# Performance work log

Hardware: AMD Instinct MI355X
Metric: run time of the kernel (lower is better)

Reference implementation:

```python
import jax, jax.numpy as jnp
import numpy as np

Nc, Np = 100_000, 200_000
E = 1_000_000
D_IN, C, H = 64, 128, 8
D = C // H  # per-head dim = 16
NEG_SLOPE = 0.2
BN_EPS = 1e-5


def setup_inputs() -> dict:
    key = jax.random.key(0)
    ks = jax.random.split(key, 24)
    rn = lambda i, shape, s=0.05: jax.random.normal(ks[i], shape, jnp.float32) * s
    inp = {
        'x_customer': jax.random.normal(ks[0], (Nc, D_IN), jnp.float32),
        'x_product': jax.random.normal(ks[1], (Np, D_IN), jnp.float32),
        'edge_src_cp': jax.random.randint(ks[2], (E,), 0, Nc),
        'edge_dst_cp': jax.random.randint(ks[3], (E,), 0, Np),
        'edge_src_pp': jax.random.randint(ks[4], (E,), 0, Np),
        'edge_dst_pp': jax.random.randint(ks[5], (E,), 0, Np),
        # HANConv per-node-type projections
        'W_c': rn(6, (D_IN, C)), 'b_c': jnp.zeros((C,), jnp.float32),
        'W_p': rn(7, (D_IN, C)), 'b_p': jnp.zeros((C,), jnp.float32),
        # per-edge-type attention vectors [H, D]
        'a_src_cp': rn(8, (H, D), 0.2), 'a_dst_cp': rn(9, (H, D), 0.2),
        'a_src_pp': rn(10, (H, D), 0.2), 'a_dst_pp': rn(11, (H, D), 0.2),
        # semantic attention (k_lin + q)
        'Wk': rn(12, (C, C)), 'bk': jnp.zeros((C,), jnp.float32),
        'q_sem': rn(13, (C,), 0.2),
        # MLP head + BN params
        'W1': rn(14, (C, 128)), 'b1': jnp.zeros((128,), jnp.float32),
        'g1': jnp.ones((128,), jnp.float32), 'be1': jnp.zeros((128,), jnp.float32),
        'W2': rn(15, (128, 64)), 'b2': jnp.zeros((64,), jnp.float32),
        'g2': jnp.ones((64,), jnp.float32), 'be2': jnp.zeros((64,), jnp.float32),
        'W3': rn(16, (64, 1)), 'b3': jnp.zeros((1,), jnp.float32),
    }
    return inp


def _edge_type_attention(h_src, h_dst, a_src, a_dst, e_src, e_dst, n_dst):
    # h_src: [N_src, H, D]; per-node attention logits [N, H]
    al_src = jnp.sum(h_src * a_src, axis=-1)
    al_dst = jnp.sum(h_dst * a_dst, axis=-1)
    al = al_src[e_src] + al_dst[e_dst]                      # [E, H]
    al = jnp.where(al >= 0, al, NEG_SLOPE * al)             # leaky_relu
    m = jax.ops.segment_max(al, e_dst, num_segments=n_dst)  # [n_dst, H]
    m = jnp.where(jnp.isfinite(m), m, 0.0)                  # empty segments
    ex = jnp.exp(al - m[e_dst])
    s = jax.ops.segment_sum(ex, e_dst, num_segments=n_dst)
    alpha = ex / (s[e_dst] + 1e-16)                         # [E, H]
    msg = h_src[e_src] * alpha[..., None]                   # [E, H, D]
    out = jax.ops.segment_sum(msg, e_dst, num_segments=n_dst)
    return jax.nn.relu(out.reshape(n_dst, H * D))


def _bn(x, g, b):
    mu = jnp.mean(x, axis=0)
    var = jnp.var(x, axis=0)
    return g * (x - mu) * jax.lax.rsqrt(var + BN_EPS) + b


def reference(x_customer, x_product, W_c, b_c, W_p, b_p,
              a_src_cp, a_dst_cp, a_src_pp, a_dst_pp,
              Wk, bk, q_sem,
              W1, b1, g1, be1, W2, b2, g2, be2, W3, b3,
              edge_src_cp, edge_dst_cp, edge_src_pp, edge_dst_pp):
    # node-type projections -> [N, H, D]
    h_c = (x_customer @ W_c + b_c).reshape(Nc, H, D)
    h_p = (x_product @ W_p + b_p).reshape(Np, H, D)
    # per-edge-type multi-head attention into 'product_order'
    out_cp = _edge_type_attention(h_c, h_p, a_src_cp, a_dst_cp, edge_src_cp, edge_dst_cp, Np)
    out_pp = _edge_type_attention(h_p, h_p, a_src_pp, a_dst_pp, edge_src_pp, edge_dst_pp, Np)
    # semantic attention over the 2 metapaths
    outs = jnp.stack([out_cp, out_pp])                      # [2, Np, C]
    k = jnp.mean(jnp.tanh(outs @ Wk + bk), axis=1)          # [2, C]
    attn = jax.nn.softmax(jnp.sum(k * q_sem, axis=-1))      # [2]
    out = jnp.sum(attn[:, None, None] * outs, axis=0)       # [Np, C]
    # MLP head (dropout disabled; BN uses batch statistics)
    h = jax.nn.relu(_bn(out @ W1 + b1, g1, be1))
    h = jax.nn.relu(_bn(h @ W2 + b2, g2, be2))
    return jax.nn.sigmoid(h @ W3 + b3)
```

## Files before the change

### kernel.cpp

```cpp
#include <hip/hip_runtime.h>
#include <hip/hip_bf16.h>

#define NC 100000
#define NP 200000
#define NE 1000000
#define NN2 (2 * NP)
#define NBUK 391
#define ECHUNK 8192
#define NBLK_E 245
#define NTILE 3125
#define NB8 391
#define NBLK_PC 391
#define NBLK_PP 782

typedef unsigned short u16;
typedef unsigned int u32;
typedef unsigned long long u64;
typedef __attribute__((ext_vector_type(8))) short short8v;
typedef __attribute__((ext_vector_type(4))) float f32x4;

__device__ __forceinline__ float bf2f(u16 v) {
    union { u32 u; float f; } c; c.u = ((u32)v) << 16; return c.f;
}
__device__ __forceinline__ u16 f2bf(float f) {
    union { float f; u32 u; } c; c.f = f;
    u32 u = c.u;
    return (u16)((u + 0x7FFFu + ((u >> 16) & 1u)) >> 16);
}
__device__ __forceinline__ u32 pack2(float lo, float hi) {
    return (u32)f2bf(lo) | ((u32)f2bf(hi) << 16);
}
__device__ __forceinline__ float tanh_fast(float x) {
    return 1.f - 2.f / (__expf(2.f * x) + 1.f);
}
__device__ __forceinline__ short8v mk8(u32 a, u32 b, u32 c, u32 d) {
    union { u32 u[4]; short8v v; } t; t.u[0] = a; t.u[1] = b; t.u[2] = c; t.u[3] = d; return t.v;
}

__global__ __launch_bounds__(256) void proj_both(
    const float* __restrict__ x_c, const float* __restrict__ W_c, const float* __restrict__ b_c,
    const float* __restrict__ x_p, const float* __restrict__ W_p, const float* __restrict__ b_p,
    u16* __restrict__ out_c, u16* __restrict__ out_p,
    const float* __restrict__ a_cp_s,
    const float* __restrict__ a_cp_d, const float* __restrict__ a_pp_s,
    const float* __restrict__ a_pp_d,
    float* __restrict__ al_c, float* __restrict__ al_dcp,
    float* __restrict__ al_spp, float* __restrict__ al_dpp,
    const int* __restrict__ dpp, const int* __restrict__ dcp, int* __restrict__ bcnt)
{
    __shared__ alignas(16) u16 sBT[128 * 72];
    __shared__ alignas(16) u16 hTile[64 * 136];
    __shared__ float aV[3][128];
    __shared__ int hh[NBUK];
    int t = threadIdx.x;
    int py = blockIdx.y;
    int bx = blockIdx.x;

    if (py == 0 && bx >= NBLK_PC) {
        int bb = bx - NBLK_PC;
        if (bb >= NBLK_E) return;
        for (int i = t; i < NBUK; i += 256) hh[i] = 0;
        __syncthreads();
        int base = bb * ECHUNK;
        int lim = min(ECHUNK, 2 * NE - base);
        for (int i = t; i < lim; i += 256) {
            int e = base + i;
            int d2 = (e < NE) ? dpp[e] : NP + dcp[e - NE];
            atomicAdd(&hh[d2 >> 10], 1);
        }
        __syncthreads();
        for (int i = t; i < NBUK; i += 256) if (hh[i]) atomicAdd(&bcnt[i], hh[i]);
        return;
    }

    const float* x; const float* W; const float* b; u16* h; int N;
    if (py == 0) { x = x_c; W = W_c; b = b_c; h = out_c; N = NC; }
    else         { x = x_p; W = W_p; b = b_p; h = out_p; N = NP; }
    if (t < 128) {
        aV[0][t] = py ? a_cp_d[t] : a_cp_s[t];
        aV[1][t] = py ? a_pp_s[t] : 0.f;
        aV[2][t] = py ? a_pp_d[t] : 0.f;
    }
    for (int i = t; i < 128 * 8; i += 256) {
        int n = i & 127, kb = i >> 7;
        u32 p[4];
#pragma unroll
        for (int j = 0; j < 4; ++j)
            p[j] = pack2(W[(kb * 8 + 2 * j) * 128 + n], W[(kb * 8 + 2 * j + 1) * 128 + n]);
        *(uint4*)(&sBT[n * 72 + kb * 8]) = make_uint4(p[0], p[1], p[2], p[3]);
    }
    __syncthreads();
    int wave = t >> 6, lane = t & 63;
    int fr = lane & 15, fq = lane >> 4;
    const u16* pB = sBT + fr * 72 + fq * 8;
    float bv8[8];
#pragma unroll
    for (int nt = 0; nt < 8; ++nt) bv8[nt] = b[nt * 16 + fr];

    for (int ti = 0; ti < 4; ++ti) {
        size_t row0 = ((size_t)bx * 4 + ti) * 64;
        if (row0 >= (size_t)N) break;
        size_t arow = row0 + wave * 16 + fr;
        short8v afr[2];
#pragma unroll
        for (int ks = 0; ks < 2; ++ks) {
            if (arow < (size_t)N) {
                const float* xp = x + arow * 64 + ks * 32 + fq * 8;
                float4 v0 = *(const float4*)xp;
                float4 v1 = *(const float4*)(xp + 4);
                afr[ks] = mk8(pack2(v0.x, v0.y), pack2(v0.z, v0.w),
                              pack2(v1.x, v1.y), pack2(v1.z, v1.w));
            } else afr[ks] = mk8(0, 0, 0, 0);
        }
        f32x4 acc[8];
#pragma unroll
        for (int nt = 0; nt < 8; ++nt) acc[nt] = (f32x4){bv8[nt], bv8[nt], bv8[nt], bv8[nt]};
#pragma unroll
        for (int ks = 0; ks < 2; ++ks) {
#pragma unroll
            for (int nt = 0; nt < 8; ++nt) {
                short8v bv = *(const short8v*)(pB + nt * 16 * 72 + ks * 32);
                acc[nt] = __builtin_amdgcn_mfma_f32_16x16x32_bf16(afr[ks], bv, acc[nt], 0, 0, 0);
            }
        }
        size_t rbase = row0 + wave * 16 + fq * 4;
        int lrow0 = wave * 16 + fq * 4;
#pragma unroll
        for (int nt = 0; nt < 8; ++nt) {
            int col = nt * 16 + fr;
#pragma unroll
            for (int rg = 0; rg < 4; ++rg) {
                size_t rr = rbase + rg;
                u16 hv = f2bf(acc[nt][rg]);
                if (rr < (size_t)N) h[rr * 128 + col] = hv;
                hTile[(lrow0 + rg) * 136 + col] = hv;
            }
        }
        __syncthreads();
        int row = t >> 2;
        size_t grow = row0 + row;
        if (grow < (size_t)N) {
#pragma unroll
            for (int hd = t & 3; hd < 8; hd += 4) {
                const u16* hp = &hTile[row * 136 + hd * 16];
                uint4 u0_ = *(const uint4*)hp;
                uint4 u1_ = *(const uint4*)(hp + 8);
                u32 uu[8] = {u0_.x, u0_.y, u0_.z, u0_.w, u1_.x, u1_.y, u1_.z, u1_.w};
                float p0 = 0.f, p1 = 0.f, p2 = 0.f;
#pragma unroll
                for (int j = 0; j < 8; ++j) {
                    float lo = bf2f((u16)(uu[j] & 0xFFFFu));
                    float hi = bf2f((u16)(uu[j] >> 16));
                    int c = hd * 16 + 2 * j;
                    p0 += lo * aV[0][c] + hi * aV[0][c + 1];
                    p1 += lo * aV[1][c] + hi * aV[1][c + 1];
                    p2 += lo * aV[2][c] + hi * aV[2][c + 1];
                }
                if (py == 0) {
                    al_c[grow * 8 + hd] = p0;
                } else {
                    al_dcp[grow * 8 + hd] = p0;
                    al_spp[grow * 8 + hd] = p1;
                    al_dpp[grow * 8 + hd] = p2;
                }
            }
        }
        __syncthreads();
    }
}

__global__ __launch_bounds__(512) void bscan(const int* __restrict__ bcnt, int* __restrict__ bbase,
                                             int* __restrict__ bcur, int* __restrict__ row_ptr)
{
    __shared__ int s[512];
    int t = threadIdx.x;
    int v = (t < NBUK) ? bcnt[t] : 0;
    s[t] = v;
    __syncthreads();
    for (int off = 1; off < 512; off <<= 1) {
        int x = (t >= off) ? s[t - off] : 0;
        __syncthreads();
        s[t] += x;
        __syncthreads();
    }
    if (t < NBUK) { bbase[t] = s[t] - v; bcur[t] = s[t] - v; }
    if (t == 0) { bbase[NBUK] = 2 * NE; row_ptr[NN2] = 2 * NE; }
}

__global__ __launch_bounds__(256) void bplace(
    const int* __restrict__ spp, const int* __restrict__ dpp,
    const int* __restrict__ scp, const int* __restrict__ dcp,
    int* __restrict__ bcur, u64* __restrict__ pairs)
{
    __shared__ int h[NBUK];
    __shared__ int rk[NBUK];
    int t = threadIdx.x;
    for (int i = t; i < NBUK; i += 256) h[i] = 0;
    __syncthreads();
    int base = blockIdx.x * ECHUNK;
    int lim = min(ECHUNK, 2 * NE - base);
    for (int i = t; i < lim; i += 256) {
        int e = base + i;
        int d2 = (e < NE) ? dpp[e] : NP + dcp[e - NE];
        atomicAdd(&h[d2 >> 10], 1);
    }
    __syncthreads();
    for (int i = t; i < NBUK; i += 256) {
        int c = h[i];
        h[i] = c ? atomicAdd(&bcur[i], c) : 0;
        rk[i] = 0;
    }
    __syncthreads();
    for (int i = t; i < lim; i += 256) {
        int e = base + i;
        int d2, src;
        if (e < NE) { d2 = dpp[e];      src = spp[e]; }
        else        { d2 = NP + dcp[e - NE]; src = scp[e - NE]; }
        int b = d2 >> 10;
        int r = atomicAdd(&rk[b], 1);
        pairs[h[b] + r] = ((u64)(u32)d2 << 32) | (u32)src;
    }
}

__global__ __launch_bounds__(256) void bsort(
    const u64* __restrict__ pairs, const int* __restrict__ bbase,
    int* __restrict__ row_ptr, int* __restrict__ perm)
{
    __shared__ int cnt[1024];
    __shared__ int sc[256];
    int b = blockIdx.x, t = threadIdx.x;
    int beg = bbase[b], end = bbase[b + 1];
    for (int i = t; i < 1024; i += 256) cnt[i] = 0;
    __syncthreads();
    for (int i = beg + t; i < end; i += 256) {
        int d2 = (int)(pairs[i] >> 32);
        atomicAdd(&cnt[d2 & 1023], 1);
    }
    __syncthreads();
    int b4 = t * 4;
    int c0 = cnt[b4], c1 = cnt[b4 + 1], c2 = cnt[b4 + 2], c3 = cnt[b4 + 3];
    int s = c0 + c1 + c2 + c3;
    sc[t] = s;
    __syncthreads();
    for (int off = 1; off < 256; off <<= 1) {
        int x = (t >= off) ? sc[t - off] : 0;
        __syncthreads();
        sc[t] += x;
        __syncthreads();
    }
    int run = sc[t] - s;
    int o0 = run, o1 = run + c0, o2 = o1 + c1, o3 = o2 + c2;
    cnt[b4] = o0; cnt[b4 + 1] = o1; cnt[b4 + 2] = o2; cnt[b4 + 3] = o3;
    int gidx = b * 1024 + b4;
    if (gidx     < NN2) row_ptr[gidx]     = beg + o0;
    if (gidx + 1 < NN2) row_ptr[gidx + 1] = beg + o1;
    if (gidx + 2 < NN2) row_ptr[gidx + 2] = beg + o2;
    if (gidx + 3 < NN2) row_ptr[gidx + 3] = beg + o3;
    __syncthreads();
    for (int i = beg + t; i < end; i += 256) {
        u64 p = pairs[i];
        int d2 = (int)(p >> 32);
        int r = atomicAdd(&cnt[d2 & 1023], 1);
        perm[beg + r] = (int)(p & 0xFFFFFFFFull);
    }
}

__global__ __launch_bounds__(256) void gather2(
    const int* __restrict__ row_ptr, const int* __restrict__ perm,
    const float* __restrict__ als_pp, const float* __restrict__ ald_pp,
    const float* __restrict__ als_cp, const float* __restrict__ ald_cp,
    const u16* __restrict__ h_p, const u16* __restrict__ h_c,
    u16* __restrict__ r_pp, u16* __restrict__ r_cp)
{
    int d2 = blockIdx.x * 16 + (threadIdx.x >> 4);
    int lane = threadIdx.x & 63;
    int l16 = lane & 15;
    int grp = lane & 48;
    int head = l16 >> 1;
    const float* als; const float* ald; const u16* hs; u16* out; int d;
    if (d2 < NP) { d = d2;      als = als_pp; ald = ald_pp; hs = h_p; out = r_pp; }
    else         { d = d2 - NP; als = als_cp; ald = ald_cp; hs = h_c; out = r_cp; }
    int beg = row_ptr[d2], end = row_ptr[d2 + 1];
    int n = end - beg;
    float ald_h = ald[(size_t)d * 8 + head];
    float dsum = 0.f;
    float acc[8] = {0.f, 0.f, 0.f, 0.f, 0.f, 0.f, 0.f, 0.f};
    for (int base = 0; base < n; base += 16) {
        int cnt = min(16, n - base);
        int my = (base + l16 < n) ? perm[beg + base + l16] : 0;
        int src = __shfl(my, grp, 64);
        float a_next = als[(size_t)src * 8 + head];
        uint4 hv_next = *(const uint4*)(hs + (size_t)src * 128 + l16 * 8);
        for (int j = 0; j < cnt; ++j) {
            float a_cur = a_next;
            uint4 hv = hv_next;
            if (j + 1 < cnt) {
                int s2 = __shfl(my, grp + j + 1, 64);
                a_next = als[(size_t)s2 * 8 + head];
                hv_next = *(const uint4*)(hs + (size_t)s2 * 128 + l16 * 8);
            }
            float a = a_cur + ald_h;
            a = a >= 0.f ? a : 0.2f * a;
            float w = __expf(a);
            dsum += w;
            u32 uu[4] = {hv.x, hv.y, hv.z, hv.w};
#pragma unroll
            for (int q = 0; q < 4; ++q) {
                acc[2 * q]     = fmaf(bf2f((u16)(uu[q] & 0xFFFFu)), w, acc[2 * q]);
                acc[2 * q + 1] = fmaf(bf2f((u16)(uu[q] >> 16)),     w, acc[2 * q + 1]);
            }
        }
    }
    float inv = 1.f / (dsum + 1e-16f);
    uint4 o;
    o.x = pack2(fmaxf(acc[0] * inv, 0.f), fmaxf(acc[1] * inv, 0.f));
    o.y = pack2(fmaxf(acc[2] * inv, 0.f), fmaxf(acc[3] * inv, 0.f));
    o.z = pack2(fmaxf(acc[4] * inv, 0.f), fmaxf(acc[5] * inv, 0.f));
    o.w = pack2(fmaxf(acc[6] * inv, 0.f), fmaxf(acc[7] * inv, 0.f));
    *(uint4*)(out + (size_t)d * 128 + l16 * 8) = o;
}

__global__ __launch_bounds__(256) void sem_mfma(
    const u16* __restrict__ r0, const u16* __restrict__ r1,
    const float* __restrict__ Wk, const float* __restrict__ bk,
    const float* __restrict__ q, float* __restrict__ vsum)
{
    __shared__ alignas(16) u16 sBT[128 * 136];
    __shared__ float red[4][128];
    __shared__ float sq_[128];
    __shared__ float dotb[128];
    int t = threadIdx.x;
    const u16* src = blockIdx.y ? r1 : r0;
    if (t < 128) sq_[t] = q[t];
    for (int i = t; i < 128 * 16; i += 256) {
        int n = i & 127, kb = i >> 7;
        u32 p[4];
#pragma unroll
        for (int j = 0; j < 4; ++j)
            p[j] = pack2(Wk[(kb * 8 + 2 * j) * 128 + n], Wk[(kb * 8 + 2 * j + 1) * 128 + n]);
        *(uint4*)(&sBT[n * 136 + kb * 8]) = make_uint4(p[0], p[1], p[2], p[3]);
    }
    __syncthreads();
    int wave = t >> 6, lane = t & 63;
    int fr = lane & 15, fq = lane >> 4;
    const u16* pB = sBT + fr * 136 + fq * 8;
    float bkv[8];
#pragma unroll
    for (int nt = 0; nt < 8; ++nt) bkv[nt] = bk[nt * 16 + fr];
    float sacc[8] = {0.f, 0.f, 0.f, 0.f, 0.f, 0.f, 0.f, 0.f};
    for (int ti = 0; ti < 8; ++ti) {
        int tile = blockIdx.x * 8 + ti;
        if (tile >= NTILE) break;
        size_t arow = (size_t)tile * 64 + wave * 16 + fr;
        const u16* ap = src + arow * 128 + fq * 8;
        short8v afr[4];
#pragma unroll
        for (int ks = 0; ks < 4; ++ks) afr[ks] = *(const short8v*)(ap + ks * 32);
        f32x4 acc[8];
#pragma unroll
        for (int nt = 0; nt < 8; ++nt) acc[nt] = (f32x4){bkv[nt], bkv[nt], bkv[nt], bkv[nt]};
#pragma unroll
        for (int ks = 0; ks < 4; ++ks) {
#pragma unroll
            for (int nt = 0; nt < 8; ++nt) {
                short8v bv = *(const short8v*)(pB + nt * 16 * 136 + ks * 32);
                acc[nt] = __builtin_amdgcn_mfma_f32_16x16x32_bf16(afr[ks], bv, acc[nt], 0, 0, 0);
            }
        }
#pragma unroll
        for (int nt = 0; nt < 8; ++nt) {
            f32x4 v = acc[nt];
            sacc[nt] += tanh_fast(v[0]) + tanh_fast(v[1]) + tanh_fast(v[2]) + tanh_fast(v[3]);
        }
    }
#pragma unroll
    for (int nt = 0; nt < 8; ++nt) {
        float s = sacc[nt];
        s += __shfl_xor(s, 16, 64);
        s += __shfl_xor(s, 32, 64);
        if (lane < 16) red[wave][nt * 16 + lane] = s;
    }
    __syncthreads();
    if (t < 128) dotb[t] = (red[0][t] + red[1][t] + red[2][t] + red[3][t]) * sq_[t];
    __syncthreads();
    if (t < 64) {
        float v = dotb[t] + dotb[t + 64];
#pragma unroll
        for (int off = 32; off >= 1; off >>= 1) v += __shfl_xor(v, off, 64);
        if (t == 0) atomicAdd(&vsum[blockIdx.y], v);
    }
}

__global__ __launch_bounds__(256) void mlp1_mfma(
    const u16* __restrict__ rcp, const u16* __restrict__ rpp, const float* __restrict__ vsum,
    const float* __restrict__ W1, const float* __restrict__ b1,
    u16* __restrict__ z1, float* __restrict__ pS, float* __restrict__ pQ)
{
    __shared__ alignas(16) u16 sBT[128 * 136];
    __shared__ float redS[4][128];
    __shared__ float redQ[4][128];
    int t = threadIdx.x;
    float v0 = vsum[0] * (1.f / (float)NP), v1 = vsum[1] * (1.f / (float)NP);
    float mx = fmaxf(v0, v1);
    float e0 = __expf(v0 - mx), e1 = __expf(v1 - mx);
    float is = 1.f / (e0 + e1);
    float a0 = e0 * is, a1 = e1 * is;
    for (int i = t; i < 128 * 16; i += 256) {
        int n = i & 127, kb = i >> 7;
        u32 p[4];
#pragma unroll
        for (int j = 0; j < 4; ++j)
            p[j] = pack2(W1[(kb * 8 + 2 * j) * 128 + n], W1[(kb * 8 + 2 * j + 1) * 128 + n]);
        *(uint4*)(&sBT[n * 136 + kb * 8]) = make_uint4(p[0], p[1], p[2], p[3]);
    }
    __syncthreads();
    int wave = t >> 6, lane = t & 63;
    int fr = lane & 15, fq = lane >> 4;
    const u16* pB = sBT + fr * 136 + fq * 8;
    float b1v[8];
#pragma unroll
    for (int nt = 0; nt < 8; ++nt) b1v[nt] = b1[nt * 16 + fr];
    float saccS[8] = {0.f, 0.f, 0.f, 0.f, 0.f, 0.f, 0.f, 0.f};
    float saccQ[8] = {0.f, 0.f, 0.f, 0.f, 0.f, 0.f, 0.f, 0.f};
    for (int ti = 0; ti < 8; ++ti) {
        int tile = blockIdx.x * 8 + ti;
        if (tile >= NTILE) break;
        size_t row0 = (size_t)tile * 64;
        size_t arow = row0 + wave * 16 + fr;
        const u16* rc = rcp + arow * 128 + fq * 8;
        const u16* rp = rpp + arow * 128 + fq * 8;
        f32x4 acc[8];
#pragma unroll
        for (int nt = 0; nt < 8; ++nt) acc[nt] = (f32x4){b1v[nt], b1v[nt], b1v[nt], b1v[nt]};
#pragma unroll
        for (int ks = 0; ks < 4; ++ks) {
            uint4 uc = *(const uint4*)(rc + ks * 32);
            uint4 up = *(const uint4*)(rp + ks * 32);
            u32 cu[4] = {uc.x, uc.y, uc.z, uc.w};
            u32 pu[4] = {up.x, up.y, up.z, up.w};
            u32 pw[4];
#pragma unroll
            for (int j = 0; j < 4; ++j) {
                float lo = a0 * bf2f((u16)(cu[j] & 0xFFFFu)) + a1 * bf2f((u16)(pu[j] & 0xFFFFu));
                float hi = a0 * bf2f((u16)(cu[j] >> 16))     + a1 * bf2f((u16)(pu[j] >> 16));
                pw[j] = pack2(lo, hi);
            }
            short8v a = mk8(pw[0], pw[1], pw[2], pw[3]);
#pragma unroll
            for (int nt = 0; nt < 8; ++nt) {
                short8v bv = *(const short8v*)(pB + nt * 16 * 136 + ks * 32);
                acc[nt] = __builtin_amdgcn_mfma_f32_16x16x32_bf16(a, bv, acc[nt], 0, 0, 0);
            }
        }
        size_t rbase = row0 + wave * 16 + fq * 4;
#pragma unroll
        for (int nt = 0; nt < 8; ++nt) {
            f32x4 v = acc[nt];
            int col = nt * 16 + fr;
#pragma unroll
            for (int rg = 0; rg < 4; ++rg)
                z1[(rbase + rg) * 128 + col] = f2bf(v[rg]);
            saccS[nt] += v[0] + v[1] + v[2] + v[3];
            saccQ[nt] += v[0] * v[0] + v[1] * v[1] + v[2] * v[2] + v[3] * v[3];
        }
    }
#pragma unroll
    for (int nt = 0; nt < 8; ++nt) {
        float s = saccS[nt], qq = saccQ[nt];
        s += __shfl_xor(s, 16, 64);  s += __shfl_xor(s, 32, 64);
        qq += __shfl_xor(qq, 16, 64); qq += __shfl_xor(qq, 32, 64);
        if (lane < 16) { redS[wave][nt * 16 + lane] = s; redQ[wave][nt * 16 + lane] = qq; }
    }
    __syncthreads();
    if (t < 128) {
        pS[(size_t)blockIdx.x * 128 + t] = redS[0][t] + redS[1][t] + redS[2][t] + redS[3][t];
        pQ[(size_t)blockIdx.x * 128 + t] = redQ[0][t] + redQ[1][t] + redQ[2][t] + redQ[3][t];
    }
}

__global__ __launch_bounds__(256) void stat_reduce(
    const float* __restrict__ pS, const float* __restrict__ pQ,
    float* __restrict__ sum, float* __restrict__ sq, int C)
{
    __shared__ float redS[256], redQ[256];
    int t = threadIdx.x;
    int c = t & (C - 1);
    int sub = t / C;
    int stride = 256 / C;
    int i0 = blockIdx.x * 25, i1 = i0 + 25;
    if (i1 > NB8) i1 = NB8;
    float s = 0.f, q = 0.f;
    for (int i = i0 + sub; i < i1; i += stride) {
        s += pS[(size_t)i * C + c];
        q += pQ[(size_t)i * C + c];
    }
    redS[t] = s; redQ[t] = q;
    __syncthreads();
    if (t < C) {
        for (int k = 1; k < stride; ++k) { s += redS[t + k * C]; q += redQ[t + k * C]; }
        atomicAdd(&sum[c], s);
        atomicAdd(&sq[c], q);
    }
}

__global__ __launch_bounds__(256) void mlp2_mfma(
    const u16* __restrict__ z1,
    const float* __restrict__ sum1, const float* __restrict__ sq1,
    const float* __restrict__ g1, const float* __restrict__ be1,
    const float* __restrict__ W2, const float* __restrict__ b2,
    u16* __restrict__ z2, float* __restrict__ pS, float* __restrict__ pQ)
{
    __shared__ alignas(16) u16 sBT[64 * 136];
    __shared__ float sSc[128], sSh[128];
    __shared__ float redS[4][64], redQ[4][64];
    int t = threadIdx.x;
    if (t < 128) {
        float mu = sum1[t] * (1.f / (float)NP);
        float var = sq1[t] * (1.f / (float)NP) - mu * mu;
        float sc = g1[t] * rsqrtf(var + 1e-5f);
        sSc[t] = sc;
        sSh[t] = be1[t] - mu * sc;
    }
    for (int i = t; i < 64 * 16; i += 256) {
        int n = i & 63, kb = i >> 6;
        u32 p[4];
#pragma unroll
        for (int j = 0; j < 4; ++j)
            p[j] = pack2(W2[(kb * 8 + 2 * j) * 64 + n], W2[(kb * 8 + 2 * j + 1) * 64 + n]);
        *(uint4*)(&sBT[n * 136 + kb * 8]) = make_uint4(p[0], p[1], p[2], p[3]);
    }
    __syncthreads();
    int wave = t >> 6, lane = t & 63;
    int fr = lane & 15, fq = lane >> 4;
    const u16* pB = sBT + fr * 136 + fq * 8;
    float b2v[4];
#pragma unroll
    for (int nt = 0; nt < 4; ++nt) b2v[nt] = b2[nt * 16 + fr];
    float saccS[4] = {0.f, 0.f, 0.f, 0.f};
    float saccQ[4] = {0.f, 0.f, 0.f, 0.f};
    for (int ti = 0; ti < 8; ++ti) {
        int tile = blockIdx.x * 8 + ti;
        if (tile >= NTILE) break;
        size_t row0 = (size_t)tile * 64;
        size_t arow = row0 + wave * 16 + fr;
        const u16* zp = z1 + arow * 128 + fq * 8;
        f32x4 acc[4];
#pragma unroll
        for (int nt = 0; nt < 4; ++nt) acc[nt] = (f32x4){b2v[nt], b2v[nt], b2v[nt], b2v[nt]};
#pragma unroll
        for (int ks = 0; ks < 4; ++ks) {
            uint4 uz = *(const uint4*)(zp + ks * 32);
            u32 zu[4] = {uz.x, uz.y, uz.z, uz.w};
            u32 pw[4];
            int c0 = ks * 32 + fq * 8;
#pragma unroll
            for (int j = 0; j < 4; ++j) {
                int c = c0 + 2 * j;
                float lo = fmaxf(bf2f((u16)(zu[j] & 0xFFFFu)) * sSc[c] + sSh[c], 0.f);
                float hi = fmaxf(bf2f((u16)(zu[j] >> 16)) * sSc[c + 1] + sSh[c + 1], 0.f);
                pw[j] = pack2(lo, hi);
            }
            short8v a = mk8(pw[0], pw[1], pw[2], pw[3]);
#pragma unroll
            for (int nt = 0; nt < 4; ++nt) {
                short8v bv = *(const short8v*)(pB + nt * 16 * 136 + ks * 32);
                acc[nt] = __builtin_amdgcn_mfma_f32_16x16x32_bf16(a, bv, acc[nt], 0, 0, 0);
            }
        }
        size_t rbase = row0 + wave * 16 + fq * 4;
#pragma unroll
        for (int nt = 0; nt < 4; ++nt) {
            f32x4 v = acc[nt];
            int col = nt * 16 + fr;
#pragma unroll
            for (int rg = 0; rg < 4; ++rg)
                z2[(rbase + rg) * 64 + col] = f2bf(v[rg]);
            saccS[nt] += v[0] + v[1] + v[2] + v[3];
            saccQ[nt] += v[0] * v[0] + v[1] * v[1] + v[2] * v[2] + v[3] * v[3];
        }
    }
#pragma unroll
    for (int nt = 0; nt < 4; ++nt) {
        float s = saccS[nt], qq = saccQ[nt];
        s += __shfl_xor(s, 16, 64);  s += __shfl_xor(s, 32, 64);
        qq += __shfl_xor(qq, 16, 64); qq += __shfl_xor(qq, 32, 64);
        if (lane < 16) { redS[wave][nt * 16 + lane] = s; redQ[wave][nt * 16 + lane] = qq; }
    }
    __syncthreads();
    if (t < 64) {
        pS[(size_t)blockIdx.x * 64 + t] = redS[0][t] + redS[1][t] + redS[2][t] + redS[3][t];
        pQ[(size_t)blockIdx.x * 64 + t] = redQ[0][t] + redQ[1][t] + redQ[2][t] + redQ[3][t];
    }
}

__global__ __launch_bounds__(64) void final_kernel(
    const u16* __restrict__ z2,
    const float* __restrict__ sum2, const float* __restrict__ sq2,
    const float* __restrict__ g2, const float* __restrict__ be2,
    const float* __restrict__ W3, const float* __restrict__ b3, float* __restrict__ out)
{
    __shared__ float sh[64][65];
    __shared__ float sw[64];
    int t = threadIdx.x;
    float mu = sum2[t] * (1.f / (float)NP);
    float var = sq2[t] * (1.f / (float)NP) - mu * mu;
    float sc = g2[t] * rsqrtf(var + 1e-5f);
    float sh2 = be2[t] - mu * sc;
    size_t row0 = (size_t)blockIdx.x * 64;
    sw[t] = W3[t];
    for (int j = 0; j < 64; ++j) {
        float v = bf2f(z2[(row0 + j) * 64 + t]) * sc + sh2;
        sh[j][t] = v > 0.f ? v : 0.f;
    }
    __syncthreads();
    float acc = b3[0];
#pragma unroll 16
    for (int k = 0; k < 64; ++k) acc = fmaf(sh[t][k], sw[k], acc);
    out[row0 + t] = 1.f / (1.f + __expf(-acc));
}

extern "C" void kernel_launch(void* const* d_in, const int* in_sizes, int n_in,
                              void* d_out, int out_size, void* d_ws, size_t ws_size,
                              hipStream_t stream) {
    const float* x_c      = (const float*)d_in[0];
    const float* x_p      = (const float*)d_in[1];
    const int*   e_src_cp = (const int*)d_in[2];
    const int*   e_dst_cp = (const int*)d_in[3];
    const int*   e_src_pp = (const int*)d_in[4];
    const int*   e_dst_pp = (const int*)d_in[5];
    const float* W_c      = (const float*)d_in[6];
    const float* b_c      = (const float*)d_in[7];
    const float* W_p      = (const float*)d_in[8];
    const float* b_p      = (const float*)d_in[9];
    const float* a_src_cp = (const float*)d_in[10];
    const float* a_dst_cp = (const float*)d_in[11];
    const float* a_src_pp = (const float*)d_in[12];
    const float* a_dst_pp = (const float*)d_in[13];
    const float* Wk       = (const float*)d_in[14];
    const float* bk       = (const float*)d_in[15];
    const float* q_sem    = (const float*)d_in[16];
    const float* W1       = (const float*)d_in[17];
    const float* b1       = (const float*)d_in[18];
    const float* g1       = (const float*)d_in[19];
    const float* be1      = (const float*)d_in[20];
    const float* W2       = (const float*)d_in[21];
    const float* b2       = (const float*)d_in[22];
    const float* g2       = (const float*)d_in[23];
    const float* be2      = (const float*)d_in[24];
    const float* W3       = (const float*)d_in[25];
    const float* b3       = (const float*)d_in[26];

    char* ws = (char*)d_ws;
    u16*   h_p    = (u16*)  (ws +          0);
    u16*   h_c    = (u16*)  (ws +  51200000);
    float* al_c   = (float*)(ws +  76800000);
    float* al_dcp = (float*)(ws +  80000000);
    float* al_spp = (float*)(ws +  86400000);
    float* al_dpp = (float*)(ws +  92800000);
    int*   row_ptr= (int*)  (ws +  99200000);
    int*   perm   = (int*)  (ws + 100800256);
    u64*   pairs  = (u64*)  (ws + 108800256);
    int*   bcnt   = (int*)  (ws + 124800256);
    int*   bbase  = (int*)  (ws + 124801856);
    int*   bcur   = (int*)  (ws + 124803456);
    u16*   r_pp   = (u16*)  (ws + 108800256);
    u16*   r_cp   = (u16*)  (ws + 160000256);
    float* small  = (float*)(ws + 211200256);

    float* statS  = (float*)(ws + 102400000);
    float* statQ  = (float*)(ws + 104000000);

    float* vsum   = small;
    float* sum1   = small + 128;
    float* sq1    = small + 256;
    float* sum2   = small + 384;
    float* sq2    = small + 448;

    u16*   z1 = h_p;
    u16*   z2 = (u16*)(ws + 51200000);

    hipMemsetAsync(small, 0, 8192, stream);
    hipMemsetAsync(bcnt, 0, 1600, stream);

    {
        dim3 g(NBLK_PP, 2);
        proj_both<<<g, 256, 0, stream>>>(x_c, W_c, b_c, x_p, W_p, b_p, h_c, h_p,
                                         a_src_cp, a_dst_cp, a_src_pp, a_dst_pp,
                                         al_c, al_dcp, al_spp, al_dpp,
                                         e_dst_pp, e_dst_cp, bcnt);
    }

    bscan<<<1, 512, 0, stream>>>(bcnt, bbase, bcur, row_ptr);
    bplace<<<NBLK_E, 256, 0, stream>>>(e_src_pp, e_dst_pp, e_src_cp, e_dst_cp, bcur, pairs);
    bsort<<<NBUK, 256, 0, stream>>>(pairs, bbase, row_ptr, perm);

    gather2<<<NN2 / 16, 256, 0, stream>>>(row_ptr, perm,
                                          al_spp, al_dpp, al_c, al_dcp,
                                          h_p, h_c, r_pp, r_cp);

    {
        dim3 gs(NB8, 2);
        sem_mfma<<<gs, 256, 0, stream>>>(r_cp, r_pp, Wk, bk, q_sem, vsum);
    }

    mlp1_mfma<<<NB8, 256, 0, stream>>>(r_cp, r_pp, vsum, W1, b1, z1, statS, statQ);
    stat_reduce<<<16, 256, 0, stream>>>(statS, statQ, sum1, sq1, 128);
    mlp2_mfma<<<NB8, 256, 0, stream>>>(z1, sum1, sq1, g1, be1, W2, b2, z2, statS, statQ);
    stat_reduce<<<16, 256, 0, stream>>>(statS, statQ, sum2, sq2, 64);
    final_kernel<<<NP / 64, 64, 0, stream>>>(z2, sum2, sq2, g2, be2, W3, b3, (float*)d_out);
}
```

Baseline: 366.5 us.

## Fold scan and stat-reduce kernels into consumers and coarsen projection blocks

Removes the separate bucket-scan kernel by having each bplace and bsort block recompute the prefix sum of bucket counts redundantly in shared memory. The two stat_reduce kernels are also removed, with mlp2 and final_kernel reducing the per-block BN partials themselves. The projection kernel now processes 8 tiles per block instead of 4, and final_kernel uses 256 threads over 4 row chunks. This cuts three launches and their serialization gaps, in exchange for redundant scan and reduction work in every block.

```diff
diff --git a/kernel.cpp b/kernel.cpp
--- a/kernel.cpp
+++ b/kernel.cpp
@@ -10,8 +10,9 @@
 #define NBLK_E 245
 #define NTILE 3125
 #define NB8 391
-#define NBLK_PC 391
-#define NBLK_PP 782
+#define NBLK_PC8 196
+#define NBLK_PP8 391
+#define GRIDX 441
 
 typedef unsigned short u16;
 typedef unsigned int u32;
@@ -56,8 +57,8 @@
     int py = blockIdx.y;
     int bx = blockIdx.x;
 
-    if (py == 0 && bx >= NBLK_PC) {
-        int bb = bx - NBLK_PC;
+    if (py == 0 && bx >= NBLK_PC8) {
+        int bb = bx - NBLK_PC8;
         if (bb >= NBLK_E) return;
         for (int i = t; i < NBUK; i += 256) hh[i] = 0;
         __syncthreads();
@@ -76,6 +77,7 @@
     const float* x; const float* W; const float* b; u16* h; int N;
     if (py == 0) { x = x_c; W = W_c; b = b_c; h = out_c; N = NC; }
     else         { x = x_p; W = W_p; b = b_p; h = out_p; N = NP; }
+    if ((size_t)bx * 512 >= (size_t)N) return;
     if (t < 128) {
         aV[0][t] = py ? a_cp_d[t] : a_cp_s[t];
         aV[1][t] = py ? a_pp_s[t] : 0.f;
@@ -97,8 +99,8 @@
 #pragma unroll
     for (int nt = 0; nt < 8; ++nt) bv8[nt] = b[nt * 16 + fr];
 
-    for (int ti = 0; ti < 4; ++ti) {
-        size_t row0 = ((size_t)bx * 4 + ti) * 64;
+    for (int ti = 0; ti < 8; ++ti) {
+        size_t row0 = ((size_t)bx * 8 + ti) * 64;
         if (row0 >= (size_t)N) break;
         size_t arow = row0 + wave * 16 + fr;
         short8v afr[2];
@@ -169,34 +171,23 @@
     }
 }
 
-__global__ __launch_bounds__(512) void bscan(const int* __restrict__ bcnt, int* __restrict__ bbase,
-                                             int* __restrict__ bcur, int* __restrict__ row_ptr)
-{
-    __shared__ int s[512];
-    int t = threadIdx.x;
-    int v = (t < NBUK) ? bcnt[t] : 0;
-    s[t] = v;
-    __syncthreads();
-    for (int off = 1; off < 512; off <<= 1) {
-        int x = (t >= off) ? s[t - off] : 0;
-        __syncthreads();
-        s[t] += x;
-        __syncthreads();
-    }
-    if (t < NBUK) { bbase[t] = s[t] - v; bcur[t] = s[t] - v; }
-    if (t == 0) { bbase[NBUK] = 2 * NE; row_ptr[NN2] = 2 * NE; }
-}
-
 __global__ __launch_bounds__(256) void bplace(
     const int* __restrict__ spp, const int* __restrict__ dpp,
     const int* __restrict__ scp, const int* __restrict__ dcp,
-    int* __restrict__ bcur, u64* __restrict__ pairs)
+    const int* __restrict__ bcnt, int* __restrict__ gcur, u64* __restrict__ pairs)
 {
+    __shared__ int sbA[NBUK], sbB[NBUK];
     __shared__ int h[NBUK];
     __shared__ int rk[NBUK];
     int t = threadIdx.x;
-    for (int i = t; i < NBUK; i += 256) h[i] = 0;
-    __syncthreads();
+    for (int i = t; i < NBUK; i += 256) { sbA[i] = bcnt[i]; h[i] = 0; }
+    __syncthreads();
+    int* cur = sbA; int* nxt = sbB;
+    for (int off = 1; off < NBUK; off <<= 1) {
+        for (int i = t; i < NBUK; i += 256) nxt[i] = cur[i] + (i >= off ? cur[i - off] : 0);
+        __syncthreads();
+        int* tmp = cur; cur = nxt; nxt = tmp;
+    }
     int base = blockIdx.x * ECHUNK;
     int lim = min(ECHUNK, 2 * NE - base);
     for (int i = t; i < lim; i += 256) {
@@ -207,7 +198,10 @@
     __syncthreads();
     for (int i = t; i < NBUK; i += 256) {
         int c = h[i];
-        h[i] = c ? atomicAdd(&bcur[i], c) : 0;
+        if (c) {
+            int excl = cur[i] - bcnt[i];
+            h[i] = excl + atomicAdd(&gcur[i], c);
+        }
         rk[i] = 0;
     }
     __syncthreads();
@@ -223,15 +217,25 @@
 }
 
 __global__ __launch_bounds__(256) void bsort(
-    const u64* __restrict__ pairs, const int* __restrict__ bbase,
+    const u64* __restrict__ pairs, const int* __restrict__ bcnt,
     int* __restrict__ row_ptr, int* __restrict__ perm)
 {
+    __shared__ int sbA[NBUK], sbB[NBUK];
     __shared__ int cnt[1024];
     __shared__ int sc[256];
     int b = blockIdx.x, t = threadIdx.x;
-    int beg = bbase[b], end = bbase[b + 1];
+    for (int i = t; i < NBUK; i += 256) sbA[i] = bcnt[i];
     for (int i = t; i < 1024; i += 256) cnt[i] = 0;
     __syncthreads();
+    int* cur = sbA; int* nxt = sbB;
+    for (int off = 1; off < NBUK; off <<= 1) {
+        for (int i = t; i < NBUK; i += 256) nxt[i] = cur[i] + (i >= off ? cur[i - off] : 0);
+        __syncthreads();
+        int* tmp = cur; cur = nxt; nxt = tmp;
+    }
+    int end = cur[b];
+    int beg = end - bcnt[b];
+    if (b == 0 && t == 0) row_ptr[NN2] = 2 * NE;
     for (int i = beg + t; i < end; i += 256) {
         int d2 = (int)(pairs[i] >> 32);
         atomicAdd(&cnt[d2 & 1023], 1);
@@ -478,34 +482,9 @@
     }
 }
 
-__global__ __launch_bounds__(256) void stat_reduce(
-    const float* __restrict__ pS, const float* __restrict__ pQ,
-    float* __restrict__ sum, float* __restrict__ sq, int C)
-{
-    __shared__ float redS[256], redQ[256];
-    int t = threadIdx.x;
-    int c = t & (C - 1);
-    int sub = t / C;
-    int stride = 256 / C;
-    int i0 = blockIdx.x * 25, i1 = i0 + 25;
-    if (i1 > NB8) i1 = NB8;
-    float s = 0.f, q = 0.f;
-    for (int i = i0 + sub; i < i1; i += stride) {
-        s += pS[(size_t)i * C + c];
-        q += pQ[(size_t)i * C + c];
-    }
-    redS[t] = s; redQ[t] = q;
-    __syncthreads();
-    if (t < C) {
-        for (int k = 1; k < stride; ++k) { s += redS[t + k * C]; q += redQ[t + k * C]; }
-        atomicAdd(&sum[c], s);
-        atomicAdd(&sq[c], q);
-    }
-}
-
 __global__ __launch_bounds__(256) void mlp2_mfma(
     const u16* __restrict__ z1,
-    const float* __restrict__ sum1, const float* __restrict__ sq1,
+    const float* __restrict__ statS1, const float* __restrict__ statQ1,
     const float* __restrict__ g1, const float* __restrict__ be1,
     const float* __restrict__ W2, const float* __restrict__ b2,
     u16* __restrict__ z2, float* __restrict__ pS, float* __restrict__ pQ)
@@ -513,21 +492,34 @@
     __shared__ alignas(16) u16 sBT[64 * 136];
     __shared__ float sSc[128], sSh[128];
     __shared__ float redS[4][64], redQ[4][64];
+    __shared__ float rs[256], rq[256];
     int t = threadIdx.x;
+    {
+        int c = t & 127, half = t >> 7;
+        float s = 0.f, q = 0.f;
+        for (int i = half; i < NB8; i += 2) {
+            s += statS1[i * 128 + c];
+            q += statQ1[i * 128 + c];
+        }
+        rs[t] = s; rq[t] = q;
+    }
+    for (int i = t; i < 64 * 16; i += 256) {
+        int n = i & 63, kb = i >> 6;
+        u32 p[4];
+#pragma unroll
+        for (int j = 0; j < 4; ++j)
+            p[j] = pack2(W2[(kb * 8 + 2 * j) * 64 + n], W2[(kb * 8 + 2 * j + 1) * 64 + n]);
+        *(uint4*)(&sBT[n * 136 + kb * 8]) = make_uint4(p[0], p[1], p[2], p[3]);
+    }
+    __syncthreads();
     if (t < 128) {
-        float mu = sum1[t] * (1.f / (float)NP);
-        float var = sq1[t] * (1.f / (float)NP) - mu * mu;
+        float s = rs[t] + rs[t + 128];
+        float q = rq[t] + rq[t + 128];
+        float mu = s * (1.f / (float)NP);
+        float var = q * (1.f / (float)NP) - mu * mu;
         float sc = g1[t] * rsqrtf(var + 1e-5f);
         sSc[t] = sc;
         sSh[t] = be1[t] - mu * sc;
-    }
-    for (int i = t; i < 64 * 16; i += 256) {
-        int n = i & 63, kb = i >> 6;
-        u32 p[4];
-#pragma unroll
-        for (int j = 0; j < 4; ++j)
-            p[j] = pack2(W2[(kb * 8 + 2 * j) * 64 + n], W2[(kb * 8 + 2 * j + 1) * 64 + n]);
-        *(uint4*)(&sBT[n * 136 + kb * 8]) = make_uint4(p[0], p[1], p[2], p[3]);
     }
     __syncthreads();
     int wave = t >> 6, lane = t & 63;
@@ -593,30 +585,56 @@
     }
 }
 
-__global__ __launch_bounds__(64) void final_kernel(
+__global__ __launch_bounds__(256) void final_kernel(
     const u16* __restrict__ z2,
-    const float* __restrict__ sum2, const float* __restrict__ sq2,
+    const float* __restrict__ statS2, const float* __restrict__ statQ2,
     const float* __restrict__ g2, const float* __restrict__ be2,
     const float* __restrict__ W3, const float* __restrict__ b3, float* __restrict__ out)
 {
     __shared__ float sh[64][65];
     __shared__ float sw[64];
+    __shared__ float sSc[64], sSh2[64];
+    __shared__ float rs[256], rq[256];
     int t = threadIdx.x;
-    float mu = sum2[t] * (1.f / (float)NP);
-    float var = sq2[t] * (1.f / (float)NP) - mu * mu;
-    float sc = g2[t] * rsqrtf(var + 1e-5f);
-    float sh2 = be2[t] - mu * sc;
-    size_t row0 = (size_t)blockIdx.x * 64;
-    sw[t] = W3[t];
-    for (int j = 0; j < 64; ++j) {
-        float v = bf2f(z2[(row0 + j) * 64 + t]) * sc + sh2;
-        sh[j][t] = v > 0.f ? v : 0.f;
-    }
-    __syncthreads();
-    float acc = b3[0];
+    {
+        int c = t & 63, sub = t >> 6;
+        float s = 0.f, q = 0.f;
+        for (int i = sub; i < NB8; i += 4) {
+            s += statS2[i * 64 + c];
+            q += statQ2[i * 64 + c];
+        }
+        rs[t] = s; rq[t] = q;
+    }
+    __syncthreads();
+    if (t < 64) {
+        float s = rs[t] + rs[t + 64] + rs[t + 128] + rs[t + 192];
+        float q = rq[t] + rq[t + 64] + rq[t + 128] + rq[t + 192];
+        float mu = s * (1.f / (float)NP);
+        float var = q * (1.f / (float)NP) - mu * mu;
+        float sc = g2[t] * rsqrtf(var + 1e-5f);
+        sSc[t] = sc;
+        sSh2[t] = be2[t] - mu * sc;
+        sw[t] = W3[t];
+    }
+    __syncthreads();
+    float b3v = b3[0];
+    for (int ch = 0; ch < 4; ++ch) {
+        size_t row0 = ((size_t)blockIdx.x * 4 + ch) * 64;
+        if (row0 >= (size_t)NP) break;
+        for (int e = t; e < 4096; e += 256) {
+            int r = e >> 6, cc = e & 63;
+            float v = bf2f(z2[(row0 + r) * 64 + cc]) * sSc[cc] + sSh2[cc];
+            sh[r][cc] = v > 0.f ? v : 0.f;
+        }
+        __syncthreads();
+        if (t < 64) {
+            float acc = b3v;
 #pragma unroll 16
-    for (int k = 0; k < 64; ++k) acc = fmaf(sh[t][k], sw[k], acc);
-    out[row0 + t] = 1.f / (1.f + __expf(-acc));
+            for (int k = 0; k < 64; ++k) acc = fmaf(sh[t][k], sw[k], acc);
+            out[row0 + t] = 1.f / (1.f + __expf(-acc));
+        }
+        __syncthreads();
+    }
 }
 
 extern "C" void kernel_launch(void* const* d_in, const int* in_sizes, int n_in,
@@ -660,39 +678,34 @@
     int*   row_ptr= (int*)  (ws +  99200000);
     int*   perm   = (int*)  (ws + 100800256);
     u64*   pairs  = (u64*)  (ws + 108800256);
-    int*   bcnt   = (int*)  (ws + 124800256);
-    int*   bbase  = (int*)  (ws + 124801856);
-    int*   bcur   = (int*)  (ws + 124803456);
     u16*   r_pp   = (u16*)  (ws + 108800256);
     u16*   r_cp   = (u16*)  (ws + 160000256);
     float* small  = (float*)(ws + 211200256);
 
-    float* statS  = (float*)(ws + 102400000);
-    float* statQ  = (float*)(ws + 104000000);
+    float* statS1 = (float*)(ws + 102400000);
+    float* statQ1 = (float*)(ws + 102600448);
+    float* statS2 = (float*)(ws + 102800896);
+    float* statQ2 = (float*)(ws + 102901248);
 
     float* vsum   = small;
-    float* sum1   = small + 128;
-    float* sq1    = small + 256;
-    float* sum2   = small + 384;
-    float* sq2    = small + 448;
+    int*   bcnt   = (int*)(small + 128);
+    int*   gcur   = (int*)(small + 640);
 
     u16*   z1 = h_p;
     u16*   z2 = (u16*)(ws + 51200000);
 
     hipMemsetAsync(small, 0, 8192, stream);
-    hipMemsetAsync(bcnt, 0, 1600, stream);
 
     {
-        dim3 g(NBLK_PP, 2);
+        dim3 g(GRIDX, 2);
         proj_both<<<g, 256, 0, stream>>>(x_c, W_c, b_c, x_p, W_p, b_p, h_c, h_p,
                                          a_src_cp, a_dst_cp, a_src_pp, a_dst_pp,
                                          al_c, al_dcp, al_spp, al_dpp,
                                          e_dst_pp, e_dst_cp, bcnt);
     }
 
-    bscan<<<1, 512, 0, stream>>>(bcnt, bbase, bcur, row_ptr);
-    bplace<<<NBLK_E, 256, 0, stream>>>(e_src_pp, e_dst_pp, e_src_cp, e_dst_cp, bcur, pairs);
-    bsort<<<NBUK, 256, 0, stream>>>(pairs, bbase, row_ptr, perm);
+    bplace<<<NBLK_E, 256, 0, stream>>>(e_src_pp, e_dst_pp, e_src_cp, e_dst_cp, bcnt, gcur, pairs);
+    bsort<<<NBUK, 256, 0, stream>>>(pairs, bcnt, row_ptr, perm);
 
     gather2<<<NN2 / 16, 256, 0, stream>>>(row_ptr, perm,
                                           al_spp, al_dpp, al_c, al_dcp,
@@ -703,9 +716,7 @@
         sem_mfma<<<gs, 256, 0, stream>>>(r_cp, r_pp, Wk, bk, q_sem, vsum);
     }
 
-    mlp1_mfma<<<NB8, 256, 0, stream>>>(r_cp, r_pp, vsum, W1, b1, z1, statS, statQ);
-    stat_reduce<<<16, 256, 0, stream>>>(statS, statQ, sum1, sq1, 128);
-    mlp2_mfma<<<NB8, 256, 0, stream>>>(z1, sum1, sq1, g1, be1, W2, b2, z2, statS, statQ);
-    stat_reduce<<<16, 256, 0, stream>>>(statS, statQ, sum2, sq2, 64);
-    final_kernel<<<NP / 64, 64, 0, stream>>>(z2, sum2, sq2, g2, be2, W3, b3, (float*)d_out);
-}
+    mlp1_mfma<<<NB8, 256, 0, stream>>>(r_cp, r_pp, vsum, W1, b1, z1, statS1, statQ1);
+    mlp2_mfma<<<NB8, 256, 0, stream>>>(z1, statS1, statQ1, g1, be1, W2, b2, z2, statS2, statQ2);
+    final_kernel<<<782, 256, 0, stream>>>(z2, statS2, statQ2, g2, be2, W3, b3, (float*)d_out);
+}
```

Result: slower. 449.0 us (+22.5%).
